# Performance work log

Hardware: AMD Instinct MI355X
Metric: run time of the kernel (lower is better)

## Reference

```python
import jax, jax.numpy as jnp
import numpy as np

N_EMBD = 768
N_HEAD = 12


def setup_inputs() -> dict:
    key = jax.random.key(0)
    ks = jax.random.split(key, 5)
    B, T, C = 2, 4096, N_EMBD
    s = 1.0 / np.sqrt(C)
    x = jax.random.normal(ks[0], (B, T, C), dtype=jnp.float32)
    w_attn = jax.random.normal(ks[1], (C, 3 * C), dtype=jnp.float32) * s
    b_attn = jnp.zeros((3 * C,), dtype=jnp.float32)
    w_proj = jax.random.normal(ks[2], (C, C), dtype=jnp.float32) * s
    b_proj = jnp.zeros((C,), dtype=jnp.float32)
    return {"x": x, "w_attn": w_attn, "b_attn": b_attn,
            "w_proj": w_proj, "b_proj": b_proj}


def reference(x, w_attn, b_attn, w_proj, b_proj):
    B, T, C = x.shape
    H = N_HEAD
    D = C // H  # head dim
    qkv = x @ w_attn + b_attn  # [B,T,3C]
    q, k, v = jnp.split(qkv, 3, axis=-1)
    # [B,H,T,D]
    q = q.reshape(B, T, H, D).transpose(0, 2, 1, 3)
    k = k.reshape(B, T, H, D).transpose(0, 2, 1, 3)
    v = v.reshape(B, T, H, D).transpose(0, 2, 1, 3)
    scale = 1.0 / jnp.sqrt(jnp.asarray(D, dtype=x.dtype))
    att = jnp.einsum('bhqd,bhkd->bhqk', q, k) * scale  # [B,H,T,T]
    causal = jnp.tril(jnp.ones((T, T), dtype=bool))
    att = jnp.where(causal[None, None], att, -jnp.inf)
    att = jax.nn.softmax(att, axis=-1)
    y = jnp.einsum('bhqk,bhkd->bhqd', att, v)  # [B,H,T,D]
    y = y.transpose(0, 2, 1, 3).reshape(B, T, C)
    return y @ w_proj + b_proj
```

## Files before the change

kernel.cpp:

```cpp
#include <hip/hip_runtime.h>

#define TSEQ 4096
#define CEMB 768
#define NHEAD 12

using bf16x8 = __attribute__((ext_vector_type(8))) short;
using f32x4  = __attribute__((ext_vector_type(4))) float;

#if __has_builtin(__builtin_amdgcn_exp2f)
#define EXP2(x) __builtin_amdgcn_exp2f(x)
#else
#define EXP2(x) exp2f(x)
#endif

__device__ __forceinline__ unsigned int f2bf(float f) {
    unsigned int u = __float_as_uint(f);
    return (u + 0x7fffu + ((u >> 16) & 1u)) >> 16;
}
__device__ __forceinline__ unsigned int f2bf_fast(float f) {
    return (__float_as_uint(f) + 0x8000u) >> 16;
}
__device__ __forceinline__ unsigned int cvt_pk_bf16(float lo, float hi) {
    unsigned int r;
    asm("v_cvt_pk_bf16_f32 %0, %1, %2" : "=v"(r) : "v"(lo), "v"(hi));
    return r;
}
__device__ __forceinline__ void async_cp16(void* lds, const void* g) {
    __builtin_amdgcn_global_load_lds(
        (const __attribute__((address_space(1))) void*)g,
        (__attribute__((address_space(3))) void*)lds, 16, 0, 0);
}

__global__ __launch_bounds__(256) void cvt_bf16(
    const float* __restrict__ X, unsigned short* __restrict__ Xb, int n8)
{
    int i = blockIdx.x * 256 + threadIdx.x;
    if (i >= n8) return;
    float4 a = *reinterpret_cast<const float4*>(&X[(size_t)i * 8]);
    float4 b = *reinterpret_cast<const float4*>(&X[(size_t)i * 8 + 4]);
    uint4 o;
    o.x = f2bf(a.x) | (f2bf(a.y) << 16);
    o.y = f2bf(a.z) | (f2bf(a.w) << 16);
    o.z = f2bf(b.x) | (f2bf(b.y) << 16);
    o.w = f2bf(b.z) | (f2bf(b.w) << 16);
    *reinterpret_cast<uint4*>(&Xb[(size_t)i * 8]) = o;
}

__global__ __launch_bounds__(256) void wtrans(
    const float* __restrict__ W, unsigned short* __restrict__ WT, int K, int N)
{
    __shared__ unsigned short tile[64][72];
    const int k0 = blockIdx.y * 64, n0 = blockIdx.x * 64;
    const int tid = threadIdx.x;
#pragma unroll
    for (int it = 0; it < 4; ++it) {
        int f = tid + it * 256;
        int r = f >> 4, c4 = f & 15;
        float4 v = *reinterpret_cast<const float4*>(&W[(size_t)(k0 + r) * N + n0 + c4 * 4]);
        tile[r][c4 * 4 + 0] = (unsigned short)f2bf(v.x);
        tile[r][c4 * 4 + 1] = (unsigned short)f2bf(v.y);
        tile[r][c4 * 4 + 2] = (unsigned short)f2bf(v.z);
        tile[r][c4 * 4 + 3] = (unsigned short)f2bf(v.w);
    }
    __syncthreads();
#pragma unroll
    for (int it = 0; it < 2; ++it) {
        int f = tid + it * 256;
        int rn = f >> 3, c8 = f & 7;
        unsigned short tmp[8];
#pragma unroll
        for (int j = 0; j < 8; ++j) tmp[j] = tile[c8 * 8 + j][rn];
        *reinterpret_cast<uint4*>(&WT[(size_t)(n0 + rn) * K + k0 + c8 * 8]) =
            *reinterpret_cast<uint4*>(tmp);
    }
}

template<int BF16OUT, int QSCALE>
__global__ __launch_bounds__(256) void gemm_mfma(
    const unsigned short* __restrict__ A,
    const unsigned short* __restrict__ BT,
    const float* __restrict__ bias,
    void* __restrict__ Cv,
    int M, int N, int K)
{
    __shared__ __align__(16) unsigned short As[128 * 64];
    __shared__ __align__(16) unsigned short Bs[128 * 64];

    const int nwg = gridDim.x * gridDim.y;
    const int id = blockIdx.y * gridDim.x + blockIdx.x;
    const int qx = nwg >> 3;
    const int swz = (id & 7) * qx + (id >> 3);
    const int nb = N >> 7;
    const int m0 = (swz / nb) * 128, n0 = (swz % nb) * 128;

    const int tid = threadIdx.x;
    const int w = tid >> 6, lane = tid & 63;
    const int wr = w >> 1, wc = w & 1;
    const int lq = lane & 15, g = lane >> 4;
    const int wrOff = wr * 64, wcOff = wc * 64;

    f32x4 acc[4][4];
#pragma unroll
    for (int i = 0; i < 4; ++i)
#pragma unroll
        for (int j = 0; j < 4; ++j) acc[i][j] = (f32x4){0.f, 0.f, 0.f, 0.f};

    for (int k0 = 0; k0 < K; k0 += 64) {
#pragma unroll
        for (int it = 0; it < 4; ++it) {
            const int dbase = it * 256 + w * 64;
            const int d = dbase + lane;
            const int r = d >> 3;
            const int s = (d & 7) ^ (r & 7);
            async_cp16((char*)As + dbase * 16, A + (size_t)(m0 + r) * K + k0 + s * 8);
            async_cp16((char*)Bs + dbase * 16, BT + (size_t)(n0 + r) * K + k0 + s * 8);
        }
        __syncthreads();

#pragma unroll
        for (int kk = 0; kk < 2; ++kk) {
            bf16x8 af[4], bfr[4];
#pragma unroll
            for (int i = 0; i < 4; ++i) {
                const int ra = wrOff + i * 16 + lq;
                af[i] = *reinterpret_cast<const bf16x8*>(
                    (char*)As + ra * 128 + (((kk * 4 + g) ^ (ra & 7)) << 4));
                const int rb = wcOff + i * 16 + lq;
                bfr[i] = *reinterpret_cast<const bf16x8*>(
                    (char*)Bs + rb * 128 + (((kk * 4 + g) ^ (rb & 7)) << 4));
            }
#pragma unroll
            for (int i = 0; i < 4; ++i)
#pragma unroll
                for (int j = 0; j < 4; ++j)
                    acc[i][j] = __builtin_amdgcn_mfma_f32_16x16x32_bf16(
                        af[i], bfr[j], acc[i][j], 0, 0, 0);
        }
        __syncthreads();
    }

#pragma unroll
    for (int i = 0; i < 4; ++i)
#pragma unroll
        for (int j = 0; j < 4; ++j) {
            const int col = n0 + wcOff + j * 16 + lq;
            const float bv = bias[col];
            const float scl = (QSCALE && col < CEMB) ? 0.18033688011112042f : 1.0f;
#pragma unroll
            for (int rg = 0; rg < 4; ++rg) {
                const int row = m0 + wrOff + i * 16 + g * 4 + rg;
                const float v = (acc[i][j][rg] + bv) * scl;
                if (BF16OUT)
                    ((unsigned short*)Cv)[(size_t)row * N + col] = (unsigned short)f2bf(v);
                else
                    ((float*)Cv)[(size_t)row * N + col] = v;
            }
        }
}

__global__ __launch_bounds__(256) void vtrans(
    const unsigned short* __restrict__ qkvB, unsigned short* __restrict__ VtG)
{
    __shared__ unsigned short tile[64][66];
    const int t0 = blockIdx.x * 64;
    const int bh = blockIdx.y;
    const int b = bh / NHEAD, h = bh % NHEAD;
    const size_t rowBase = (size_t)b * TSEQ;
    const int tid = threadIdx.x;

#pragma unroll
    for (int it = 0; it < 2; ++it) {
        int f = tid + 256 * it;
        int r = f >> 3, s = f & 7;
        unsigned short tmp[8];
        *reinterpret_cast<uint4*>(tmp) = *reinterpret_cast<const uint4*>(
            &qkvB[(rowBase + t0 + r) * 2304 + 2 * CEMB + h * 64 + s * 8]);
#pragma unroll
        for (int j = 0; j < 8; ++j) tile[r][s * 8 + j] = tmp[j];
    }
    __syncthreads();
#pragma unroll
    for (int it = 0; it < 2; ++it) {
        int f = tid + 256 * it;
        int d = f >> 3, c = f & 7;
        unsigned short tmp[8];
#pragma unroll
        for (int j = 0; j < 8; ++j) tmp[j] = tile[c * 8 + j][d];
        *reinterpret_cast<uint4*>(&VtG[(size_t)bh * 64 * TSEQ + (size_t)d * TSEQ + t0 + c * 8]) =
            *reinterpret_cast<uint4*>(tmp);
    }
}


#define QK_DUAL(SA, SB)                                                               \
{                                                                                     \
    const int xr = lq & 7;                                                            \
    _Pragma("unroll")                                                                 \
    for (int c = 0; c < 4; ++c) {                                                     \
        const int krow = 16 * c + lq;                                                 \
        bf16x8 kf0 = *reinterpret_cast<const bf16x8*>(Kb + krow * 128 + ((g ^ xr) << 4));       \
        bf16x8 kf1 = *reinterpret_cast<const bf16x8*>(Kb + krow * 128 + (((4 + g) ^ xr) << 4)); \
        f32x4 a = (f32x4){0.f, 0.f, 0.f, 0.f};                                        \
        a = __builtin_amdgcn_mfma_f32_16x16x32_bf16(kf0, qfA[0], a, 0, 0, 0);         \
        a = __builtin_amdgcn_mfma_f32_16x16x32_bf16(kf1, qfA[1], a, 0, 0, 0);         \
        SA[c] = a;                                                                    \
        f32x4 bb = (f32x4){0.f, 0.f, 0.f, 0.f};                                       \
        bb = __builtin_amdgcn_mfma_f32_16x16x32_bf16(kf0, qfB[0], bb, 0, 0, 0);       \
        bb = __builtin_amdgcn_mfma_f32_16x16x32_bf16(kf1, qfB[1], bb, 0, 0, 0);       \
        SB[c] = bb;                                                                   \
    }                                                                                 \
}

#define QK_ONE(SB, QF)                                                                \
{                                                                                     \
    const int xr = lq & 7;                                                            \
    _Pragma("unroll")                                                                 \
    for (int c = 0; c < 4; ++c) {                                                     \
        const int krow = 16 * c + lq;                                                 \
        bf16x8 kf0 = *reinterpret_cast<const bf16x8*>(Kb + krow * 128 + ((g ^ xr) << 4));       \
        bf16x8 kf1 = *reinterpret_cast<const bf16x8*>(Kb + krow * 128 + (((4 + g) ^ xr) << 4)); \
        f32x4 a = (f32x4){0.f, 0.f, 0.f, 0.f};                                        \
        a = __builtin_amdgcn_mfma_f32_16x16x32_bf16(kf0, QF[0], a, 0, 0, 0);          \
        a = __builtin_amdgcn_mfma_f32_16x16x32_bf16(kf1, QF[1], a, 0, 0, 0);          \
        SB[c] = a;                                                                    \
    }                                                                                 \
}

#define MASK_TILE(SFR)                                                                \
{                                                                                     \
    const int qloc = 16 * w + lq;                                                     \
    _Pragma("unroll")                                                                 \
    for (int c = 0; c < 4; ++c)                                                       \
        _Pragma("unroll")                                                             \
        for (int r = 0; r < 4; ++r)                                                   \
            if (16 * c + 4 * g + r > qloc) SFR[c][r] = -1e30f;                        \
}

#define SM_TILE(SFR, MM, LL, OO)                                                      \
{                                                                                     \
    float mx = SFR[0][0];                                                             \
    _Pragma("unroll")                                                                 \
    for (int c = 0; c < 4; ++c)                                                       \
        _Pragma("unroll")                                                             \
        for (int r = 0; r < 4; ++r) mx = fmaxf(mx, SFR[c][r]);                        \
    mx = fmaxf(mx, __shfl_xor(mx, 16));                                               \
    mx = fmaxf(mx, __shfl_xor(mx, 32));                                               \
    const float mnew = fmaxf(MM, mx);                                                 \
    const float al = EXP2(MM - mnew);                                                 \
    MM = mnew;                                                                        \
    float rs = 0.f;                                                                   \
    _Pragma("unroll")                                                                 \
    for (int c = 0; c < 4; ++c)                                                       \
        _Pragma("unroll")                                                             \
        for (int r = 0; r < 4; ++r) {                                                 \
            const float p = EXP2(SFR[c][r] - mnew);                                   \
            SFR[c][r] = p;                                                            \
            rs += p;                                                                  \
        }                                                                             \
    rs += __shfl_xor(rs, 16);                                                         \
    rs += __shfl_xor(rs, 32);                                                         \
    LL = al * LL + rs;                                                                \
    _Pragma("unroll")                                                                 \
    for (int dt = 0; dt < 4; ++dt) OO[dt] *= al;                                      \
}

#define PW_TILE(SFR, PWP)                                                             \
{                                                                                     \
    _Pragma("unroll")                                                                 \
    for (int c = 0; c < 4; ++c) {                                                     \
        uint2 pk;                                                                     \
        pk.x = cvt_pk_bf16(SFR[c][0], SFR[c][1]);                                     \
        pk.y = cvt_pk_bf16(SFR[c][2], SFR[c][3]);                                     \
        *reinterpret_cast<uint2*>(PWP + lq * 128 +                                    \
            (((2 * c + (g >> 1)) ^ (lq & 7)) << 4) + (g & 1) * 8) = pk;               \
    }                                                                                 \
}

#define PV_DUAL(OA, OB, PWA, PWB)                                                     \
{                                                                                     \
    const int xq = lq & 7;                                                            \
    bf16x8 pA0 = *reinterpret_cast<const bf16x8*>(PWA + lq * 128 + ((g ^ xq) << 4));       \
    bf16x8 pA1 = *reinterpret_cast<const bf16x8*>(PWA + lq * 128 + (((4 + g) ^ xq) << 4)); \
    bf16x8 pB0 = *reinterpret_cast<const bf16x8*>(PWB + lq * 128 + ((g ^ xq) << 4));       \
    bf16x8 pB1 = *reinterpret_cast<const bf16x8*>(PWB + lq * 128 + (((4 + g) ^ xq) << 4)); \
    _Pragma("unroll")                                                                 \
    for (int dt = 0; dt < 4; ++dt) {                                                  \
        const int vrow = 16 * dt + lq;                                                \
        bf16x8 vf0 = *reinterpret_cast<const bf16x8*>(Vb + vrow * 128 + ((g ^ xq) << 4));       \
        bf16x8 vf1 = *reinterpret_cast<const bf16x8*>(Vb + vrow * 128 + (((4 + g) ^ xq) << 4)); \
        OA[dt] = __builtin_amdgcn_mfma_f32_16x16x32_bf16(vf0, pA0, OA[dt], 0, 0, 0);  \
        OA[dt] = __builtin_amdgcn_mfma_f32_16x16x32_bf16(vf1, pA1, OA[dt], 0, 0, 0);  \
        OB[dt] = __builtin_amdgcn_mfma_f32_16x16x32_bf16(vf0, pB0, OB[dt], 0, 0, 0);  \
        OB[dt] = __builtin_amdgcn_mfma_f32_16x16x32_bf16(vf1, pB1, OB[dt], 0, 0, 0);  \
    }                                                                                 \
}

#define PV_ONE(OB, PWB)                                                               \
{                                                                                     \
    const int xq = lq & 7;                                                            \
    bf16x8 pB0 = *reinterpret_cast<const bf16x8*>(PWB + lq * 128 + ((g ^ xq) << 4));       \
    bf16x8 pB1 = *reinterpret_cast<const bf16x8*>(PWB + lq * 128 + (((4 + g) ^ xq) << 4)); \
    _Pragma("unroll")                                                                 \
    for (int dt = 0; dt < 4; ++dt) {                                                  \
        const int vrow = 16 * dt + lq;                                                \
        bf16x8 vf0 = *reinterpret_cast<const bf16x8*>(Vb + vrow * 128 + ((g ^ xq) << 4));       \
        bf16x8 vf1 = *reinterpret_cast<const bf16x8*>(Vb + vrow * 128 + (((4 + g) ^ xq) << 4)); \
        OB[dt] = __builtin_amdgcn_mfma_f32_16x16x32_bf16(vf0, pB0, OB[dt], 0, 0, 0);  \
        OB[dt] = __builtin_amdgcn_mfma_f32_16x16x32_bf16(vf1, pB1, OB[dt], 0, 0, 0);  \
    }                                                                                 \
}

#define STAGE_KV(KT, BUF)                                                             \
{                                                                                     \
    const int kn = (KT) * 64;                                                         \
    _Pragma("unroll")                                                                 \
    for (int it = 0; it < 2; ++it) {                                                  \
        const int dbase = it * 256 + w * 64;                                          \
        const int d = dbase + lane;                                                   \
        const int r = d >> 3;                                                         \
        const int s = (d & 7) ^ (r & 7);                                              \
        async_cp16(Kl[BUF] + dbase * 16, qkvB + (rowBase + kn + r) * 2304 + kOff + s * 8); \
        async_cp16(Vl[BUF] + dbase * 16, Vhead + (size_t)r * TSEQ + kn + s * 8);      \
    }                                                                                 \
}

__global__ __launch_bounds__(256, 3) void attn_mfma8(
    const unsigned short* __restrict__ qkvB,
    const unsigned short* __restrict__ VtG,
    unsigned short* __restrict__ Yb)
{
    __shared__ __align__(16) char Kl[2][8192];
    __shared__ __align__(16) char Vl[2][8192];
    __shared__ __align__(16) char PlA[8192];
    __shared__ __align__(16) char PlB[8192];

    const int NT = TSEQ / 64;
    const int id = blockIdx.x;
    const int xcd = id & 7;
    const int local = id >> 3;
    const int bh = xcd * 3 + (local % 3);
    const int qtA = local / 3;
    const int qtB = NT - 1 - qtA;

    const int b = bh / NHEAD, h = bh % NHEAD;
    const int tid = threadIdx.x;
    const int w = tid >> 6, lane = tid & 63;
    const int g = lane >> 4, lq = lane & 15;

    const size_t rowBase = (size_t)b * TSEQ;
    const int kOff = CEMB + h * 64;
    const unsigned short* Vhead = VtG + (size_t)bh * 64 * TSEQ;

    bf16x8 qfA[2], qfB[2];
    {
        const size_t rA = rowBase + (size_t)qtA * 64 + 16 * w + lq;
        const size_t rB = rowBase + (size_t)qtB * 64 + 16 * w + lq;
#pragma unroll
        for (int dt = 0; dt < 2; ++dt) {
            qfA[dt] = *reinterpret_cast<const bf16x8*>(&qkvB[rA * 2304 + h * 64 + 32 * dt + 8 * g]);
            qfB[dt] = *reinterpret_cast<const bf16x8*>(&qkvB[rB * 2304 + h * 64 + 32 * dt + 8 * g]);
        }
    }

    f32x4 oA[4], oB[4];
    float mA = -1e30f, lA = 0.f, mB = -1e30f, lB = 0.f;
#pragma unroll
    for (int dt = 0; dt < 4; ++dt) {
        oA[dt] = (f32x4){0.f, 0.f, 0.f, 0.f};
        oB[dt] = (f32x4){0.f, 0.f, 0.f, 0.f};
    }

    char* PwA = PlA + w * 2048;
    char* PwB = PlB + w * 2048;

    STAGE_KV(0, 0);

    for (int kt = 0; kt <= qtA; ++kt) {
        const int cur = kt & 1;
        __syncthreads();
        STAGE_KV(kt + 1, cur ^ 1);
        const char* Kb = Kl[cur];
        const char* Vb = Vl[cur];

        f32x4 sA[4], sB[4];
        QK_DUAL(sA, sB);
        if (kt == qtA) MASK_TILE(sA);
        SM_TILE(sA, mA, lA, oA);
        SM_TILE(sB, mB, lB, oB);
        PW_TILE(sA, PwA);
        PW_TILE(sB, PwB);
        PV_DUAL(oA, oB, PwA, PwB);
    }

    for (int kt = qtA + 1; kt <= qtB; ++kt) {
        const int cur = kt & 1;
        __syncthreads();
        if (kt < qtB) STAGE_KV(kt + 1, cur ^ 1);
        const char* Kb = Kl[cur];
        const char* Vb = Vl[cur];

        f32x4 sB[4];
        QK_ONE(sB, qfB);
        if (kt == qtB) MASK_TILE(sB);
        SM_TILE(sB, mB, lB, oB);
        PW_TILE(sB, PwB);
        PV_ONE(oB, PwB);
    }

    const float invA = 1.f / lA;
    const float invB = 1.f / lB;
    const size_t rowA = rowBase + (size_t)qtA * 64 + 16 * w + lq;
    const size_t rowB = rowBase + (size_t)qtB * 64 + 16 * w + lq;
#pragma unroll
    for (int dt = 0; dt < 4; ++dt) {
        uint2 a, bb;
        a.x  = f2bf_fast(oA[dt][0] * invA) | (f2bf_fast(oA[dt][1] * invA) << 16);
        a.y  = f2bf_fast(oA[dt][2] * invA) | (f2bf_fast(oA[dt][3] * invA) << 16);
        bb.x = f2bf_fast(oB[dt][0] * invB) | (f2bf_fast(oB[dt][1] * invB) << 16);
        bb.y = f2bf_fast(oB[dt][2] * invB) | (f2bf_fast(oB[dt][3] * invB) << 16);
        *reinterpret_cast<uint2*>(&Yb[rowA * CEMB + h * 64 + 16 * dt + 4 * g]) = a;
        *reinterpret_cast<uint2*>(&Yb[rowB * CEMB + h * 64 + 16 * dt + 4 * g]) = bb;
    }
}

extern "C" void kernel_launch(void* const* d_in, const int* in_sizes, int n_in,
                              void* d_out, int out_size, void* d_ws, size_t ws_size,
                              hipStream_t stream)
{
    const float* x      = (const float*)d_in[0];
    const float* w_attn = (const float*)d_in[1];
    const float* b_attn = (const float*)d_in[2];
    const float* w_proj = (const float*)d_in[3];
    const float* b_proj = (const float*)d_in[4];
    float* out = (float*)d_out;

    const int M = 2 * TSEQ;
    char* ws = (char*)d_ws;
    unsigned short* qkvB = (unsigned short*)ws;
    unsigned short* VtG  = (unsigned short*)(ws + 37748736);
    unsigned short* xYb  = (unsigned short*)(ws + 50331648);
    unsigned short* wT   = (unsigned short*)(ws + 62914560);
    unsigned short* wpT  = (unsigned short*)(ws + 66453504);

    cvt_bf16<<<dim3((M * CEMB) / 8 / 256), 256, 0, stream>>>(x, xYb, (M * CEMB) / 8);
    wtrans<<<dim3(3 * CEMB / 64, CEMB / 64), 256, 0, stream>>>(w_attn, wT, CEMB, 3 * CEMB);
    wtrans<<<dim3(CEMB / 64, CEMB / 64), 256, 0, stream>>>(w_proj, wpT, CEMB, CEMB);

    gemm_mfma<1, 1><<<dim3(3 * CEMB / 128, M / 128), 256, 0, stream>>>(
        xYb, wT, b_attn, qkvB, M, 3 * CEMB, CEMB);

    vtrans<<<dim3(TSEQ / 64, 2 * NHEAD), 256, 0, stream>>>(qkvB, VtG);

    attn_mfma8<<<dim3(768), 256, 0, stream>>>(qkvB, VtG, xYb);

    gemm_mfma<0, 0><<<dim3(CEMB / 128, M / 128), 256, 0, stream>>>(
        xYb, wpT, b_proj, out, M, CEMB, CEMB);
}
```

Baseline: 183.5 us.

## Fuse V transpose into QKV GEMM epilogue and single-buffer K for occupancy

The QKV GEMM epilogue now writes the V columns directly in transposed per-head layout, which removes the separate vtrans kernel and its extra pass over V. The attention kernel keeps only one K buffer in LDS (V stays double-buffered) and raises launch bounds to 4 blocks per CU. This adds a second barrier per iteration so K can be restaged after QK. The risks are scattered 8-byte transposed stores in the GEMM epilogue and less overlap of the K loads.

```diff
diff --git a/kernel.cpp b/kernel.cpp
--- a/kernel.cpp
+++ b/kernel.cpp
@@ -75,12 +75,13 @@
     }
 }
 
-template<int BF16OUT, int QSCALE>
+template<int BF16OUT, int QSCALE, int VTRANS>
 __global__ __launch_bounds__(256) void gemm_mfma(
     const unsigned short* __restrict__ A,
     const unsigned short* __restrict__ BT,
     const float* __restrict__ bias,
     void* __restrict__ Cv,
+    unsigned short* __restrict__ VtG,
     int M, int N, int K)
 {
     __shared__ __align__(16) unsigned short As[128 * 64];
@@ -146,49 +147,34 @@
             const int col = n0 + wcOff + j * 16 + lq;
             const float bv = bias[col];
             const float scl = (QSCALE && col < CEMB) ? 0.18033688011112042f : 1.0f;
-#pragma unroll
-            for (int rg = 0; rg < 4; ++rg) {
-                const int row = m0 + wrOff + i * 16 + g * 4 + rg;
-                const float v = (acc[i][j][rg] + bv) * scl;
-                if (BF16OUT)
-                    ((unsigned short*)Cv)[(size_t)row * N + col] = (unsigned short)f2bf(v);
-                else
-                    ((float*)Cv)[(size_t)row * N + col] = v;
+            const int row0 = m0 + wrOff + i * 16 + g * 4;
+            float v0 = (acc[i][j][0] + bv) * scl;
+            float v1 = (acc[i][j][1] + bv) * scl;
+            float v2 = (acc[i][j][2] + bv) * scl;
+            float v3 = (acc[i][j][3] + bv) * scl;
+            if (VTRANS && col >= 2 * CEMB) {
+                const int hh = (col - 2 * CEMB) >> 6;
+                const int dd = col & 63;
+                uint2 pk;
+                pk.x = f2bf(v0) | (f2bf(v1) << 16);
+                pk.y = f2bf(v2) | (f2bf(v3) << 16);
+                *reinterpret_cast<uint2*>(
+                    &VtG[((size_t)(row0 >> 12) * NHEAD + hh) * 64 * TSEQ +
+                         (size_t)dd * TSEQ + (row0 & 4095)]) = pk;
+            } else if (BF16OUT) {
+                unsigned short* Cb = (unsigned short*)Cv;
+                Cb[(size_t)(row0 + 0) * N + col] = (unsigned short)f2bf(v0);
+                Cb[(size_t)(row0 + 1) * N + col] = (unsigned short)f2bf(v1);
+                Cb[(size_t)(row0 + 2) * N + col] = (unsigned short)f2bf(v2);
+                Cb[(size_t)(row0 + 3) * N + col] = (unsigned short)f2bf(v3);
+            } else {
+                float* Cf = (float*)Cv;
+                Cf[(size_t)(row0 + 0) * N + col] = v0;
+                Cf[(size_t)(row0 + 1) * N + col] = v1;
+                Cf[(size_t)(row0 + 2) * N + col] = v2;
+                Cf[(size_t)(row0 + 3) * N + col] = v3;
             }
         }
-}
-
-__global__ __launch_bounds__(256) void vtrans(
-    const unsigned short* __restrict__ qkvB, unsigned short* __restrict__ VtG)
-{
-    __shared__ unsigned short tile[64][66];
-    const int t0 = blockIdx.x * 64;
-    const int bh = blockIdx.y;
-    const int b = bh / NHEAD, h = bh % NHEAD;
-    const size_t rowBase = (size_t)b * TSEQ;
-    const int tid = threadIdx.x;
-
-#pragma unroll
-    for (int it = 0; it < 2; ++it) {
-        int f = tid + 256 * it;
-        int r = f >> 3, s = f & 7;
-        unsigned short tmp[8];
-        *reinterpret_cast<uint4*>(tmp) = *reinterpret_cast<const uint4*>(
-            &qkvB[(rowBase + t0 + r) * 2304 + 2 * CEMB + h * 64 + s * 8]);
-#pragma unroll
-        for (int j = 0; j < 8; ++j) tile[r][s * 8 + j] = tmp[j];
-    }
-    __syncthreads();
-#pragma unroll
-    for (int it = 0; it < 2; ++it) {
-        int f = tid + 256 * it;
-        int d = f >> 3, c = f & 7;
-        unsigned short tmp[8];
-#pragma unroll
-        for (int j = 0; j < 8; ++j) tmp[j] = tile[c * 8 + j][d];
-        *reinterpret_cast<uint4*>(&VtG[(size_t)bh * 64 * TSEQ + (size_t)d * TSEQ + t0 + c * 8]) =
-            *reinterpret_cast<uint4*>(tmp);
-    }
 }
 
 
@@ -310,7 +296,7 @@
     }                                                                                 \
 }
 
-#define STAGE_KV(KT, BUF)                                                             \
+#define STAGE_K(KT)                                                                   \
 {                                                                                     \
     const int kn = (KT) * 64;                                                         \
     _Pragma("unroll")                                                                 \
@@ -319,17 +305,29 @@
         const int d = dbase + lane;                                                   \
         const int r = d >> 3;                                                         \
         const int s = (d & 7) ^ (r & 7);                                              \
-        async_cp16(Kl[BUF] + dbase * 16, qkvB + (rowBase + kn + r) * 2304 + kOff + s * 8); \
+        async_cp16(Kl + dbase * 16, qkvB + (rowBase + kn + r) * 2304 + kOff + s * 8); \
+    }                                                                                 \
+}
+
+#define STAGE_V(KT, BUF)                                                              \
+{                                                                                     \
+    const int kn = (KT) * 64;                                                         \
+    _Pragma("unroll")                                                                 \
+    for (int it = 0; it < 2; ++it) {                                                  \
+        const int dbase = it * 256 + w * 64;                                          \
+        const int d = dbase + lane;                                                   \
+        const int r = d >> 3;                                                         \
+        const int s = (d & 7) ^ (r & 7);                                              \
         async_cp16(Vl[BUF] + dbase * 16, Vhead + (size_t)r * TSEQ + kn + s * 8);      \
     }                                                                                 \
 }
 
-__global__ __launch_bounds__(256, 3) void attn_mfma8(
+__global__ __launch_bounds__(256, 4) void attn_mfma9(
     const unsigned short* __restrict__ qkvB,
     const unsigned short* __restrict__ VtG,
     unsigned short* __restrict__ Yb)
 {
-    __shared__ __align__(16) char Kl[2][8192];
+    __shared__ __align__(16) char Kl[8192];
     __shared__ __align__(16) char Vl[2][8192];
     __shared__ __align__(16) char PlA[8192];
     __shared__ __align__(16) char PlB[8192];
@@ -373,17 +371,20 @@
     char* PwA = PlA + w * 2048;
     char* PwB = PlB + w * 2048;
 
-    STAGE_KV(0, 0);
+    STAGE_K(0);
+    STAGE_V(0, 0);
+
+    const char* Kb = Kl;
 
     for (int kt = 0; kt <= qtA; ++kt) {
-        const int cur = kt & 1;
-        __syncthreads();
-        STAGE_KV(kt + 1, cur ^ 1);
-        const char* Kb = Kl[cur];
-        const char* Vb = Vl[cur];
-
+        __syncthreads();
         f32x4 sA[4], sB[4];
         QK_DUAL(sA, sB);
+        __syncthreads();
+        STAGE_K(kt + 1);
+        STAGE_V(kt + 1, (kt + 1) & 1);
+        const char* Vb = Vl[kt & 1];
+
         if (kt == qtA) MASK_TILE(sA);
         SM_TILE(sA, mA, lA, oA);
         SM_TILE(sB, mB, lB, oB);
@@ -393,14 +394,16 @@
     }
 
     for (int kt = qtA + 1; kt <= qtB; ++kt) {
-        const int cur = kt & 1;
-        __syncthreads();
-        if (kt < qtB) STAGE_KV(kt + 1, cur ^ 1);
-        const char* Kb = Kl[cur];
-        const char* Vb = Vl[cur];
-
+        __syncthreads();
         f32x4 sB[4];
         QK_ONE(sB, qfB);
+        __syncthreads();
+        if (kt < qtB) {
+            STAGE_K(kt + 1);
+            STAGE_V(kt + 1, (kt + 1) & 1);
+        }
+        const char* Vb = Vl[kt & 1];
+
         if (kt == qtB) MASK_TILE(sB);
         SM_TILE(sB, mB, lB, oB);
         PW_TILE(sB, PwB);
@@ -446,13 +449,11 @@
     wtrans<<<dim3(3 * CEMB / 64, CEMB / 64), 256, 0, stream>>>(w_attn, wT, CEMB, 3 * CEMB);
     wtrans<<<dim3(CEMB / 64, CEMB / 64), 256, 0, stream>>>(w_proj, wpT, CEMB, CEMB);
 
-    gemm_mfma<1, 1><<<dim3(3 * CEMB / 128, M / 128), 256, 0, stream>>>(
-        xYb, wT, b_attn, qkvB, M, 3 * CEMB, CEMB);
-
-    vtrans<<<dim3(TSEQ / 64, 2 * NHEAD), 256, 0, stream>>>(qkvB, VtG);
-
-    attn_mfma8<<<dim3(768), 256, 0, stream>>>(qkvB, VtG, xYb);
-
-    gemm_mfma<0, 0><<<dim3(CEMB / 128, M / 128), 256, 0, stream>>>(
-        xYb, wpT, b_proj, out, M, CEMB, CEMB);
-}
+    gemm_mfma<1, 1, 1><<<dim3(3 * CEMB / 128, M / 128), 256, 0, stream>>>(
+        xYb, wT, b_attn, qkvB, VtG, M, 3 * CEMB, CEMB);
+
+    attn_mfma9<<<dim3(768), 256, 0, stream>>>(qkvB, VtG, xYb);
+
+    gemm_mfma<0, 0, 0><<<dim3(CEMB / 128, M / 128), 256, 0, stream>>>(
+        xYb, wpT, b_proj, out, nullptr, M, CEMB, CEMB);
+}
```

Result: no change. 185.8 us (+1.3%).
